# Performance work log

Hardware: AMD Instinct MI355X
Metric: run time of the kernel (lower is better)

## Reference

```python
import jax, jax.numpy as jnp
import numpy as np

LN_EPS = 1e-5  # haiku LayerNorm default

def setup_inputs() -> dict:
    key = jax.random.key(0)
    ks = jax.random.split(key, 4)
    batch, width, mid = 8192, 1024, 4096
    x = jax.random.normal(ks[0], (batch, 4, width), dtype=jnp.float32)
    W1 = jax.random.normal(ks[1], (4 * width, mid), dtype=jnp.float32) / np.sqrt(4 * width)
    b1 = jnp.zeros((mid,), dtype=jnp.float32)
    W2 = jax.random.normal(ks[2], (mid, width), dtype=jnp.float32) / np.sqrt(mid)
    b2 = jnp.zeros((width,), dtype=jnp.float32)
    ln_scale = jnp.ones((width,), dtype=jnp.float32)
    ln_offset = jnp.zeros((width,), dtype=jnp.float32)
    return {"x": x, "ln_scale": ln_scale, "ln_offset": ln_offset,
            "W1": W1, "b1": b1, "W2": W2, "b2": b2}

def _layer_norm(x, scale, offset):
    mu = jnp.mean(x, axis=-1, keepdims=True)
    var = jnp.var(x, axis=-1, keepdims=True)
    return (x - mu) * jax.lax.rsqrt(var + LN_EPS) * scale + offset

def reference(x, ln_scale, ln_offset, W1, b1, W2, b2):
    batch, four, width = x.shape  # four == 4 (structural symmetry axis)
    y = _layer_norm(x, ln_scale, ln_offset)
    # rolls[b, k, j, :] = y[b, (j + k) % 4, :]; reshape concatenates along j
    rolls = jnp.stack([jnp.roll(y, -k, axis=1) for k in range(4)], axis=1)
    rolls = rolls.reshape(batch, 4, 4 * width)
    h = jnp.einsum('bkf,fm->bkm', rolls, W1) + b1  # (batch, 4, mid)
    h = jax.nn.gelu(h)  # approximate (tanh) gelu, jax default
    out = jnp.einsum('bkm,mw->bkw', h, W2) + b2  # (batch, 4, width)
    return x + out
```

## Files before the change

kernel.cpp:

```cpp
#include <hip/hip_runtime.h>
#include <hip/hip_bf16.h>
#include <cstdint>
#include <cstddef>

typedef __bf16 bf16_t;
typedef __bf16 bf16x4_v __attribute__((ext_vector_type(4)));
typedef __bf16 bf16x8_v __attribute__((ext_vector_type(8)));
typedef float  f32x4_v  __attribute__((ext_vector_type(4)));

__device__ __forceinline__ void gll16(const void* g, void* l) {
  __builtin_amdgcn_global_load_lds(
      (const __attribute__((address_space(1))) void*)g,
      (__attribute__((address_space(3))) void*)l, 16, 0, 0);
}

#define BARRIER()  asm volatile("s_barrier" ::: "memory")
#define WAIT_VM(N) asm volatile("s_waitcnt vmcnt(" #N ")" ::: "memory")

__device__ __forceinline__ float gelu_tanh(float x) {
  float z = 0.79788456080286535588f * (x + 0.044715f * x * x * x);
  return x / (1.0f + __expf(-2.0f * z));
}

__global__ __launch_bounds__(256) void ln_kernel(
    const float* __restrict__ X, const float* __restrict__ sc,
    const float* __restrict__ off, bf16_t* __restrict__ Y)
{
  const int row = blockIdx.x;
  const int tid = threadIdx.x;
  const float4 v = *(const float4*)&X[(size_t)row * 1024 + tid * 4];
  float s  = v.x + v.y + v.z + v.w;
  float s2 = v.x * v.x + v.y * v.y + v.z * v.z + v.w * v.w;
#pragma unroll
  for (int m = 1; m < 64; m <<= 1) {
    s  += __shfl_xor(s, m);
    s2 += __shfl_xor(s2, m);
  }
  __shared__ float red[8];
  const int wid = tid >> 6;
  if ((tid & 63) == 0) { red[wid] = s; red[4 + wid] = s2; }
  __syncthreads();
  s  = red[0] + red[1] + red[2] + red[3];
  s2 = red[4] + red[5] + red[6] + red[7];
  const float mu  = s * (1.0f / 1024.0f);
  float var = s2 * (1.0f / 1024.0f) - mu * mu;
  var = fmaxf(var, 0.0f);
  const float rs = rsqrtf(var + 1e-5f);
  const float4 g = *(const float4*)&sc[tid * 4];
  const float4 o = *(const float4*)&off[tid * 4];
  bf16x4_v y;
  y[0] = (bf16_t)((v.x - mu) * rs * g.x + o.x);
  y[1] = (bf16_t)((v.y - mu) * rs * g.y + o.y);
  y[2] = (bf16_t)((v.z - mu) * rs * g.z + o.z);
  y[3] = (bf16_t)((v.w - mu) * rs * g.w + o.w);
  *(bf16x4_v*)&Y[(size_t)row * 1024 + tid * 4] = y;
}

__global__ __launch_bounds__(256) void transpose_kernel(
    const float* __restrict__ Win, bf16_t* __restrict__ Wt, int R, int C)
{
  __shared__ float t[32][33];
  const int tx = threadIdx.x & 31;
  const int ty = (threadIdx.x >> 5) << 2;
  const int r0 = blockIdx.y * 32;
  const int c0 = blockIdx.x * 32;
#pragma unroll
  for (int r = 0; r < 4; ++r)
    t[ty + r][tx] = Win[(size_t)(r0 + ty + r) * C + (c0 + tx)];
  __syncthreads();
#pragma unroll
  for (int r = 0; r < 4; ++r)
    Wt[(size_t)(c0 + ty + r) * R + (r0 + tx)] = (bf16_t)t[tx][ty + r];
}


#define LOADA(DST, I0)                                                        \
  _Pragma("unroll") for (int di_ = 0; di_ < 2; ++di_) {                       \
    DST[di_][0] = *(const bf16x8_v*)(Ab + arow + ((I0) + di_) * 2048 + cs0);  \
    DST[di_][1] = *(const bf16x8_v*)(Ab + arow + ((I0) + di_) * 2048 + cs1);  \
  }

#define MFMA2(AV, I0)                                                         \
  __builtin_amdgcn_s_setprio(1);                                              \
  _Pragma("unroll") for (int di_ = 0; di_ < 2; ++di_)                         \
  _Pragma("unroll") for (int kk_ = 0; kk_ < 2; ++kk_)                         \
  _Pragma("unroll") for (int j_ = 0; j_ < 4; ++j_)                            \
    acc[(I0) + di_][j_] = __builtin_amdgcn_mfma_f32_16x16x32_bf16(            \
        AV[di_][kk_], bfrag[j_][kk_], acc[(I0) + di_][j_], 0, 0, 0);          \
  __builtin_amdgcn_s_setprio(0);

#define ISSUE_A(NB, F, Q)                                                     \
  gll16(Asrc + ((size_t)(Q) * 64 * 4096) + (size_t)(F) * 64,                  \
        (char*)(&As[NB][0]) + (Q) * 8192 + ldsdst)
#define ISSUE_B(NB, F, Q)                                                     \
  gll16(Bsrc + ((size_t)(Q) * 64 * 4096) +                                    \
            (MODE == 1 ? ((((F) * 64) + rolloff) & 4095) : ((F) * 64)),       \
        (char*)(&Bs[NB][0]) + (Q) * 8192 + ldsdst)

template<int MODE>
__global__ __launch_bounds__(512, 2) void gemm256_kernel(
    const bf16_t* __restrict__ Ag, const bf16_t* __restrict__ Bg,
    const float* __restrict__ bias, const float* __restrict__ Xres,
    void* __restrict__ Out, long rowbase)
{
  __shared__ __align__(16) bf16_t As[2][256 * 64];
  __shared__ __align__(16) bf16_t Bs[2][256 * 64];

  const int tid  = threadIdx.x;
  const int lane = tid & 63;
  const int wid  = tid >> 6;
  const int wm   = wid >> 2;
  const int wn   = wid & 3;

  const int nwgx = gridDim.x;
  const int nwg  = nwgx * gridDim.y;
  const int flat = blockIdx.y * nwgx + blockIdx.x;
  const int swz  = (flat & 7) * (nwg >> 3) + (flat >> 3);
  const int bm   = swz % nwgx;
  const int bnl  = swz / nwgx;

  int kgrp = 0, m0, rolloff = 0;
  if (MODE == 1) { kgrp = bnl >> 4; m0 = (bnl & 15) << 8; rolloff = ((4 - kgrp) & 3) << 10; }
  else           { m0 = bnl << 8; }

  const int trow = tid >> 3;
  const int scb  = (((tid & 7) ^ (trow & 7)) << 4);
  const bf16_t* Asrc = Ag + (size_t)(bm * 256 + trow) * 4096 + (scb >> 1);
  const bf16_t* Bsrc = Bg + (size_t)(m0 + trow) * 4096 + (scb >> 1);
  const int ldsdst = (wid << 10);

  const int arow = (wm * 128 + (lane & 15)) * 128;
  const int brow = (wn * 64  + (lane & 15)) * 128;
  const int cs0  = (((lane >> 4) << 4)     ) ^ ((lane & 7) << 4);
  const int cs1  = (((lane >> 4) << 4) | 64) ^ ((lane & 7) << 4);

  f32x4_v  acc[8][4] = {};
  bf16x8_v bfrag[4][2];

#pragma unroll
  for (int q = 0; q < 4; ++q) ISSUE_B(0, 0, q);
#pragma unroll
  for (int q = 0; q < 4; ++q) ISSUE_A(0, 0, q);
  WAIT_VM(0);
  BARRIER();

  int cur = 0;
  for (int f = 0; f < 64; ++f) {
    const char* Ab = (const char*)(&As[cur][0]);
    const char* Bb = (const char*)(&Bs[cur][0]);
    const int  nb = cur ^ 1;
    const bool st = (f < 63);

    {
#pragma unroll
      for (int j = 0; j < 4; ++j) {
        bfrag[j][0] = *(const bf16x8_v*)(Bb + brow + j * 2048 + cs0);
        bfrag[j][1] = *(const bf16x8_v*)(Bb + brow + j * 2048 + cs1);
      }
      bf16x8_v av[2][2];
      LOADA(av, 0);
      if (st) { ISSUE_B(nb, f + 1, 0); ISSUE_B(nb, f + 1, 1);
                ISSUE_B(nb, f + 1, 2); ISSUE_B(nb, f + 1, 3); }
      BARRIER();
      MFMA2(av, 0);
      BARRIER();
    }
    {
      bf16x8_v av[2][2];
      LOADA(av, 2);
      if (st) { ISSUE_A(nb, f + 1, 0); ISSUE_A(nb, f + 1, 2);
                ISSUE_A(nb, f + 1, 1); ISSUE_A(nb, f + 1, 3); }
      BARRIER();
      MFMA2(av, 2);
      if (st) { WAIT_VM(8); } else { WAIT_VM(0); }
      BARRIER();
    }
    {
      bf16x8_v av[2][2];
      LOADA(av, 4);
      BARRIER();
      MFMA2(av, 4);
      BARRIER();
    }
    {
      bf16x8_v av[2][2];
      LOADA(av, 6);
      BARRIER();
      MFMA2(av, 6);
      if (st) WAIT_VM(2);
      BARRIER();
    }
    cur = nb;
  }

  const int cb16 = lane & 15;
  const int r4   = (lane >> 4) << 2;
  if (MODE == 1) {
    bf16_t* H = (bf16_t*)Out;
#pragma unroll
    for (int j = 0; j < 4; ++j) {
      const int m = m0 + wn * 64 + j * 16 + cb16;
      const float bv = bias[m];
#pragma unroll
      for (int i = 0; i < 8; ++i) {
        const int browi = bm * 256 + wm * 128 + i * 16 + r4;
#pragma unroll
        for (int r = 0; r < 4; ++r) {
          float v = acc[i][j][r] + bv;
          H[((size_t)(browi + r) * 4 + kgrp) * 4096 + m] = (bf16_t)gelu_tanh(v);
        }
      }
    }
  } else {
    float* O = (float*)Out;
#pragma unroll
    for (int j = 0; j < 4; ++j) {
      const int w = m0 + wn * 64 + j * 16 + cb16;
      const float bv = bias[w];
#pragma unroll
      for (int i = 0; i < 8; ++i) {
        const long row = rowbase + bm * 256 + wm * 128 + i * 16 + r4;
#pragma unroll
        for (int r = 0; r < 4; ++r)
          O[(size_t)(row + r) * 1024 + w] =
              Xres[(size_t)(row + r) * 1024 + w] + acc[i][j][r] + bv;
      }
    }
  }
}

extern "C" void kernel_launch(void* const* d_in, const int* in_sizes, int n_in,
                              void* d_out, int out_size, void* d_ws, size_t ws_size,
                              hipStream_t stream)
{
  const float* x   = (const float*)d_in[0];
  const float* lns = (const float*)d_in[1];
  const float* lno = (const float*)d_in[2];
  const float* W1  = (const float*)d_in[3];
  const float* b1  = (const float*)d_in[4];
  const float* W2  = (const float*)d_in[5];
  const float* b2  = (const float*)d_in[6];
  float* out = (float*)d_out;

  char* ws = (char*)d_ws;
  const size_t W1OFF = (size_t)64 << 20;
  const size_t W2OFF = (size_t)96 << 20;
  const size_t HOFF  = (size_t)104 << 20;
  bf16_t* Y   = (bf16_t*)(ws);
  bf16_t* W1t = (bf16_t*)(ws + W1OFF);
  bf16_t* W2t = (bf16_t*)(ws + W2OFF);
  bf16_t* H   = (bf16_t*)(ws + HOFF);

  ln_kernel<<<32768, 256, 0, stream>>>(x, lns, lno, Y);
  transpose_kernel<<<dim3(128, 128), 256, 0, stream>>>(W1, W1t, 4096, 4096);
  transpose_kernel<<<dim3(32, 128), 256, 0, stream>>>(W2, W2t, 4096, 1024);

  const size_t per_row = (size_t)4 * 4096 * 2;
  long chunk = 8192;
  if (ws_size < HOFF + (size_t)8192 * per_row) {
    long maxb = (long)((ws_size - HOFF) / per_row);
    chunk = maxb & ~255L;
    if (chunk < 256) chunk = 256;
  }
  for (long b0 = 0; b0 < 8192; b0 += chunk) {
    const long cb = (8192 - b0 < chunk) ? (8192 - b0) : chunk;
    gemm256_kernel<1><<<dim3(cb / 256, 64), 512, 0, stream>>>(
        Y + (size_t)b0 * 4096, W1t, b1, nullptr, (void*)H, 0);
    gemm256_kernel<2><<<dim3((cb * 4) / 256, 4), 512, 0, stream>>>(
        H, W2t, b2, x, (void*)out, b0 * 4);
  }
}
```

Measured before the change: 1.472 ms.

## Restructure GEMM inner loop into 2x2 quadrant MFMA phases with staggered prefetch

Reorders the 256x256 GEMM K-step into four quadrant phases (A rows 0-3/4-7 by B cols 0-1/2-3), reusing register-held A and B fragments across phases so each LDS fragment is read once per step with fewer reads per phase. Global-to-LDS prefetches for the next tile are spread two at a time across the phases, and the wait counts are adjusted. This holds more fragment registers live (a03, a47, b01, b23), which raises register pressure, and the partial waits tighten the ordering constraints on when buffer halves become visible.

```diff
diff --git a/kernel.cpp b/kernel.cpp
--- a/kernel.cpp
+++ b/kernel.cpp
@@ -74,19 +74,25 @@
 }
 
 
-#define LOADA(DST, I0)                                                        \
-  _Pragma("unroll") for (int di_ = 0; di_ < 2; ++di_) {                       \
-    DST[di_][0] = *(const bf16x8_v*)(Ab + arow + ((I0) + di_) * 2048 + cs0);  \
-    DST[di_][1] = *(const bf16x8_v*)(Ab + arow + ((I0) + di_) * 2048 + cs1);  \
-  }
-
-#define MFMA2(AV, I0)                                                         \
+#define RD_A(DST, IB)                                                         \
+  _Pragma("unroll") for (int i4_ = 0; i4_ < 4; ++i4_) {                       \
+    DST[i4_][0] = *(const bf16x8_v*)(Ab + arow + ((IB) + i4_) * 2048 + cs0);  \
+    DST[i4_][1] = *(const bf16x8_v*)(Ab + arow + ((IB) + i4_) * 2048 + cs1);  \
+  }
+
+#define RD_B(DST, JB)                                                         \
+  _Pragma("unroll") for (int j2_ = 0; j2_ < 2; ++j2_) {                       \
+    DST[j2_][0] = *(const bf16x8_v*)(Bb + brow + ((JB) + j2_) * 2048 + cs0);  \
+    DST[j2_][1] = *(const bf16x8_v*)(Bb + brow + ((JB) + j2_) * 2048 + cs1);  \
+  }
+
+#define MFMAQ(AV, BV, I0, J0)                                                 \
   __builtin_amdgcn_s_setprio(1);                                              \
-  _Pragma("unroll") for (int di_ = 0; di_ < 2; ++di_)                         \
+  _Pragma("unroll") for (int i2_ = 0; i2_ < 4; ++i2_)                         \
+  _Pragma("unroll") for (int j2_ = 0; j2_ < 2; ++j2_)                         \
   _Pragma("unroll") for (int kk_ = 0; kk_ < 2; ++kk_)                         \
-  _Pragma("unroll") for (int j_ = 0; j_ < 4; ++j_)                            \
-    acc[(I0) + di_][j_] = __builtin_amdgcn_mfma_f32_16x16x32_bf16(            \
-        AV[di_][kk_], bfrag[j_][kk_], acc[(I0) + di_][j_], 0, 0, 0);          \
+    acc[(I0) + i2_][(J0) + j2_] = __builtin_amdgcn_mfma_f32_16x16x32_bf16(    \
+        AV[i2_][kk_], BV[j2_][kk_], acc[(I0) + i2_][(J0) + j2_], 0, 0, 0);    \
   __builtin_amdgcn_s_setprio(0);
 
 #define ISSUE_A(NB, F, Q)                                                     \
@@ -135,13 +141,11 @@
   const int cs1  = (((lane >> 4) << 4) | 64) ^ ((lane & 7) << 4);
 
   f32x4_v  acc[8][4] = {};
-  bf16x8_v bfrag[4][2];
-
-#pragma unroll
-  for (int q = 0; q < 4; ++q) ISSUE_B(0, 0, q);
-#pragma unroll
-  for (int q = 0; q < 4; ++q) ISSUE_A(0, 0, q);
-  WAIT_VM(0);
+  bf16x8_v a03[4][2], a47[4][2], b01[2][2], b23[2][2];
+
+  ISSUE_B(0, 0, 0); ISSUE_B(0, 0, 1); ISSUE_B(0, 0, 2); ISSUE_B(0, 0, 3);
+  ISSUE_A(0, 0, 0); ISSUE_A(0, 0, 2); ISSUE_A(0, 0, 1); ISSUE_A(0, 0, 3);
+  WAIT_VM(2);
   BARRIER();
 
   int cur = 0;
@@ -152,41 +156,32 @@
     const bool st = (f < 63);
 
     {
-#pragma unroll
-      for (int j = 0; j < 4; ++j) {
-        bfrag[j][0] = *(const bf16x8_v*)(Bb + brow + j * 2048 + cs0);
-        bfrag[j][1] = *(const bf16x8_v*)(Bb + brow + j * 2048 + cs1);
-      }
-      bf16x8_v av[2][2];
-      LOADA(av, 0);
-      if (st) { ISSUE_B(nb, f + 1, 0); ISSUE_B(nb, f + 1, 1);
-                ISSUE_B(nb, f + 1, 2); ISSUE_B(nb, f + 1, 3); }
-      BARRIER();
-      MFMA2(av, 0);
-      BARRIER();
-    }
-    {
-      bf16x8_v av[2][2];
-      LOADA(av, 2);
-      if (st) { ISSUE_A(nb, f + 1, 0); ISSUE_A(nb, f + 1, 2);
-                ISSUE_A(nb, f + 1, 1); ISSUE_A(nb, f + 1, 3); }
-      BARRIER();
-      MFMA2(av, 2);
-      if (st) { WAIT_VM(8); } else { WAIT_VM(0); }
-      BARRIER();
-    }
-    {
-      bf16x8_v av[2][2];
-      LOADA(av, 4);
-      BARRIER();
-      MFMA2(av, 4);
-      BARRIER();
-    }
-    {
-      bf16x8_v av[2][2];
-      LOADA(av, 6);
-      BARRIER();
-      MFMA2(av, 6);
+      RD_B(b01, 0);
+      RD_A(a03, 0);
+      if (st) { ISSUE_B(nb, f + 1, 0); ISSUE_B(nb, f + 1, 1); }
+      BARRIER();
+      MFMAQ(a03, b01, 0, 0);
+      if (st) { WAIT_VM(2); } else { WAIT_VM(0); }
+      BARRIER();
+    }
+    {
+      RD_A(a47, 4);
+      if (st) { ISSUE_B(nb, f + 1, 2); ISSUE_B(nb, f + 1, 3); }
+      BARRIER();
+      MFMAQ(a47, b01, 4, 0);
+      BARRIER();
+    }
+    {
+      RD_B(b23, 2);
+      if (st) { ISSUE_A(nb, f + 1, 0); ISSUE_A(nb, f + 1, 2); }
+      BARRIER();
+      MFMAQ(a03, b23, 0, 2);
+      BARRIER();
+    }
+    {
+      if (st) { ISSUE_A(nb, f + 1, 1); ISSUE_A(nb, f + 1, 3); }
+      BARRIER();
+      MFMAQ(a47, b23, 4, 2);
       if (st) WAIT_VM(2);
       BARRIER();
     }
```

Result: slower. 1.546 ms (+5.0%).
